# Kernel tuning notes

Hardware: AMD Instinct MI355X
Metric: run time of the kernel (lower is better)

Reference implementation:

```python
import jax, jax.numpy as jnp
import numpy as np

B, T, N_EMBD = 8, 2048, 512
N_HEAD = 4
EPS = 1e-5
NEG_INF = -1e9


def setup_inputs() -> dict:
    key = jax.random.key(0)
    ks = jax.random.split(key, 10)
    x = jax.random.normal(ks[0], (B, T, N_EMBD), dtype=jnp.float32)
    # relative-position index map [t, t] into a (2t-1)-entry boolean mask table
    pos_emb = jax.random.randint(ks[1], (T, T), 0, 2 * T - 1)
    ln_w = jax.random.normal(ks[2], (N_EMBD,), dtype=jnp.float32) * 0.02 + 1.0
    ln_b = jax.random.normal(ks[3], (N_EMBD,), dtype=jnp.float32) * 0.02
    aff_w = jax.random.normal(ks[4], (N_EMBD,), dtype=jnp.float32) * 0.02 + 1.0
    aff_b = jax.random.normal(ks[5], (N_EMBD,), dtype=jnp.float32) * 0.02
    W_qkv = jax.random.normal(ks[6], (N_EMBD, 3 * N_EMBD), dtype=jnp.float32) * (N_EMBD ** -0.5)
    # boolean lookup table; True = position visible (mostly visible)
    mask_table = jax.random.uniform(ks[7], (2 * T - 1,)) > 0.2
    W_proj = jax.random.normal(ks[8], (N_EMBD, N_EMBD), dtype=jnp.float32) * (N_EMBD ** -0.5)
    return {
        "x": x, "pos_emb": pos_emb, "ln_w": ln_w, "ln_b": ln_b,
        "aff_w": aff_w, "aff_b": aff_b, "W_qkv": W_qkv,
        "mask_table": mask_table, "W_proj": W_proj,
    }


def reference(x, pos_emb, ln_w, ln_b, aff_w, aff_b, W_qkv, mask_table, W_proj):
    b, t, n = x.shape
    hd = n // N_HEAD
    # LayerNorm (mean subtract, rms normalize, affine)
    x = x - jnp.mean(x, axis=-1, keepdims=True)
    x = x * jax.lax.rsqrt(jnp.mean(x * x, axis=-1, keepdims=True) + EPS)
    x = x * ln_w + ln_b
    # extra affine (onnx initializers 7/8) then fused QKV projection
    x = x * aff_w + aff_b
    qkv = x @ W_qkv                       # [b, t, 3n]
    q, k, v = jnp.split(qkv, 3, axis=2)
    q = q.reshape(b, t, N_HEAD, hd).transpose(0, 2, 1, 3)  # [b, h, t, hd]
    k = k.reshape(b, t, N_HEAD, hd).transpose(0, 2, 1, 3)
    v = v.reshape(b, t, N_HEAD, hd).transpose(0, 2, 1, 3)
    scale = 1.0 / np.sqrt(hd).astype(np.float32)
    scores = jnp.einsum('bhqd,bhkd->bhqk', q, k) * scale   # [b, h, t, t]
    # gather-based relative-position mask: True = attend, False = mask out
    mask = mask_table[pos_emb]                             # [t, t] bool
    scores = jnp.where(mask, scores, NEG_INF)
    attn = jax.nn.softmax(scores, axis=-1)
    out = jnp.einsum('bhqk,bhkd->bhqd', attn, v)           # [b, h, t, hd]
    out = out.transpose(0, 2, 1, 3).reshape(b, t, n)
    return out @ W_proj
```

## Files before the change

kernel.cpp:

```cpp
#include <hip/hip_runtime.h>
#include <hip/hip_bf16.h>

#define T_SEQ 2048
#define NEMBD 512
#define NHEAD 4
#define HDIM  128
#define BATCH 8
#define MROWS (BATCH * T_SEQ)
#define QSCALE 0.12751744534f

typedef __attribute__((ext_vector_type(8))) short short8;
typedef __attribute__((ext_vector_type(4))) short short4v;
typedef __attribute__((ext_vector_type(4))) float f32x4;

static __device__ __forceinline__ float bf2f(unsigned short h) {
  return __uint_as_float(((unsigned int)h) << 16);
}
static __device__ __forceinline__ short f2bs(float f) {
  unsigned int u = __float_as_uint(f);
  unsigned int r = (u + 0x7FFFu + ((u >> 16) & 1u)) >> 16;
  return (short)r;
}
static __device__ __forceinline__ unsigned int pk2(float a, float b) {
  __hip_bfloat162 h = __float22bfloat162_rn(make_float2(a, b));
  return *reinterpret_cast<unsigned int*>(&h);
}
static __device__ __forceinline__ int mask_at(const void* mt, int fmt, int idx) {
  if (fmt == 0) return ((const int*)mt)[idx] != 0;
  if (fmt == 1) return ((const unsigned char*)mt)[idx] != 0;
  if (fmt == 2) return ((const float*)mt)[idx] != 0.0f;
  return ((const unsigned short*)mt)[idx] != 0;
}
static __device__ __forceinline__ int pos_at(const int* pos, int i64, size_t idx) {
  return i64 ? pos[idx * 2] : pos[idx];
}
static __device__ __forceinline__ void gload16(const void* g, void* l) {
  __builtin_amdgcn_global_load_lds((const __attribute__((address_space(1))) void*)g,
                                   (__attribute__((address_space(3))) void*)l,
                                   16, 0, 0);
}

__global__ __launch_bounds__(256) void detect_kernel(
    const unsigned int* __restrict__ mt, const unsigned int* __restrict__ posw,
    int* __restrict__ flags)
{
  __shared__ int s01, sf, sbf, szero;
  const int t = threadIdx.x;
  if (t == 0) { s01 = 1; sf = 1; sbf = 1; szero = 0; }
  __syncthreads();
  int a01 = 1, af = 1, ab = 1, zc = 0;
  for (int i = t; i < 1023; i += 256) {
    const unsigned int v = mt[i];
    if (v > 1u) a01 = 0;
    const float f = __uint_as_float(v);
    if (!(f == 0.0f || f == 1.0f)) af = 0;
    const unsigned int lo = v & 0xFFFFu, hi = v >> 16;
    if (!((lo == 0u || lo == 0x3F80u) && (hi == 0u || hi == 0x3F80u))) ab = 0;
  }
  for (int i = t; i < 512; i += 256) if (posw[2 * i + 1] == 0u) zc++;
  if (!a01) atomicAnd(&s01, 0);
  if (!af)  atomicAnd(&sf, 0);
  if (!ab)  atomicAnd(&sbf, 0);
  if (zc)   atomicAdd(&szero, zc);
  __syncthreads();
  if (t == 0) {
    flags[0] = s01 ? 0 : (sf ? 2 : (sbf ? 3 : 1));
    flags[2] = (szero > 500) ? 1 : 0;
  }
}

__global__ __launch_bounds__(256) void pack_mask_kernel(
    const int* __restrict__ pos, const void* __restrict__ mt,
    const int* __restrict__ flags, unsigned int* __restrict__ mp)
{
  const int idx = blockIdx.x * 256 + threadIdx.x;
  const int fmt = flags[0];
  const int i64 = flags[2];
  const int q = idx >> 6;
  const int wrd = idx & 63;
  const size_t base = (size_t)q * T_SEQ + wrd * 32;
  unsigned int bits = 0;
  #pragma unroll 4
  for (int j = 0; j < 32; ++j)
    bits |= (mask_at(mt, fmt, pos_at(pos, i64, base + j)) ? 1u : 0u) << j;
  mp[idx] = bits;
}

__global__ __launch_bounds__(256) void vecprep_kernel(
    const float* __restrict__ lnw, const float* __restrict__ lnb,
    const float* __restrict__ afw, const float* __restrict__ afb,
    float* __restrict__ effw, float* __restrict__ effb)
{
  const int c = blockIdx.x * 256 + threadIdx.x;
  if (c >= NEMBD) return;
  effw[c] = lnw[c] * afw[c];
  effb[c] = lnb[c] * afw[c] + afb[c];
}

__global__ __launch_bounds__(256) void wconv2_kernel(
    const float* __restrict__ Wq, const float* __restrict__ Wp,
    short* __restrict__ WqT, short* __restrict__ WpT)
{
  const int idx = blockIdx.x * 256 + threadIdx.x;
  if (idx < 1536 * 512) {
    const int n = idx >> 9, k = idx & 511;
    WqT[idx] = f2bs(Wq[(size_t)k * 1536 + n]);
  } else {
    const int j = idx - 1536 * 512;
    const int n = j >> 9, k = j & 511;
    WpT[j] = f2bs(Wp[(size_t)k * 512 + n]);
  }
}

__global__ __launch_bounds__(64) void ln_kernel(
    const float* __restrict__ x, const float* __restrict__ effw, const float* __restrict__ effb,
    short* __restrict__ xp)
{
  const int row = blockIdx.x;
  const int tid = threadIdx.x;
  const float4* p = (const float4*)(x + (size_t)row * NEMBD + tid * 8);
  const float4 a0 = p[0], a1 = p[1];
  float f[8] = {a0.x, a0.y, a0.z, a0.w, a1.x, a1.y, a1.z, a1.w};
  float s = 0.f, s2 = 0.f;
  #pragma unroll
  for (int j = 0; j < 8; ++j) { s += f[j]; s2 += f[j] * f[j]; }
  #pragma unroll
  for (int off = 1; off < 64; off <<= 1) {
    s  += __shfl_xor(s, off);
    s2 += __shfl_xor(s2, off);
  }
  const float mean = s * (1.0f / NEMBD);
  const float rstd = rsqrtf(s2 * (1.0f / NEMBD) - mean * mean + 1e-5f);
  const float4* wp = (const float4*)(effw + tid * 8);
  const float4* bp = (const float4*)(effb + tid * 8);
  const float4 w0 = wp[0], w1 = wp[1], b0 = bp[0], b1 = bp[1];
  short8 ob;
  ob[0] = f2bs((f[0] - mean) * rstd * w0.x + b0.x);
  ob[1] = f2bs((f[1] - mean) * rstd * w0.y + b0.y);
  ob[2] = f2bs((f[2] - mean) * rstd * w0.z + b0.z);
  ob[3] = f2bs((f[3] - mean) * rstd * w0.w + b0.w);
  ob[4] = f2bs((f[4] - mean) * rstd * w1.x + b1.x);
  ob[5] = f2bs((f[5] - mean) * rstd * w1.y + b1.y);
  ob[6] = f2bs((f[6] - mean) * rstd * w1.z + b1.z);
  ob[7] = f2bs((f[7] - mean) * rstd * w1.w + b1.w);
  *((short8*)(xp + (size_t)row * NEMBD + tid * 8)) = ob;
}

template<int MODE>
__global__ __launch_bounds__(256) void gemm_kernel(
    const short* __restrict__ A, const short* __restrict__ Bt,
    void* __restrict__ out0, short* __restrict__ Kp, short* __restrict__ Vt)
{
  __shared__ alignas(16) short Atile[128 * 64];
  __shared__ alignas(16) short Btile[128 * 64];
  const int tid = threadIdx.x;
  const int l = tid & 63;
  const int w = tid >> 6;
  const int m0 = blockIdx.x * 128;
  const int n0 = blockIdx.y * 128;
  const int w_r = w >> 1, w_c = w & 1;
  const int lr = l & 15, lg = l >> 4;
  f32x4 acc[4][4] = {};

  for (int kt = 0; kt < 512; kt += 64) {
    #pragma unroll
    for (int i = 0; i < 4; ++i) {
      const int c = i * 256 + tid;
      const int row = c >> 3, col8 = c & 7;
      gload16(A  + (size_t)(m0 + row) * 512 + kt + col8 * 8, Atile + (i * 256 + w * 64) * 8);
      gload16(Bt + (size_t)(n0 + row) * 512 + kt + col8 * 8, Btile + (i * 256 + w * 64) * 8);
    }
    __syncthreads();
    #pragma unroll
    for (int kk = 0; kk < 2; ++kk) {
      short8 af[4], bfm[4];
      #pragma unroll
      for (int m = 0; m < 4; ++m)
        af[m] = *(const short8*)&Atile[(w_r * 64 + m * 16 + lr) * 64 + kk * 32 + lg * 8];
      #pragma unroll
      for (int n = 0; n < 4; ++n)
        bfm[n] = *(const short8*)&Btile[(w_c * 64 + n * 16 + lr) * 64 + kk * 32 + lg * 8];
      #pragma unroll
      for (int m = 0; m < 4; ++m)
        #pragma unroll
        for (int n = 0; n < 4; ++n)
          acc[m][n] = __builtin_amdgcn_mfma_f32_16x16x32_bf16(af[m], bfm[n], acc[m][n], 0, 0, 0);
    }
    __syncthreads();
  }

  if (MODE == 1) {
    float* out = (float*)out0;
    #pragma unroll
    for (int m = 0; m < 4; ++m)
      #pragma unroll
      for (int n = 0; n < 4; ++n)
        #pragma unroll
        for (int r = 0; r < 4; ++r) {
          const int gm = m0 + w_r * 64 + m * 16 + lg * 4 + r;
          const int gn = n0 + w_c * 64 + n * 16 + lr;
          out[(size_t)gm * NEMBD + gn] = acc[m][n][r];
        }
  } else {
    const int which = n0 >> 9;
    const int h = (n0 >> 7) & 3;
    short* Qp = (short*)out0;
    #pragma unroll
    for (int m = 0; m < 4; ++m)
      #pragma unroll
      for (int n = 0; n < 4; ++n)
        #pragma unroll
        for (int r = 0; r < 4; ++r) {
          const int gm = m0 + w_r * 64 + m * 16 + lg * 4 + r;
          const int b = gm >> 11, t = gm & 2047;
          const int d = w_c * 64 + n * 16 + lr;
          const size_t bh = (size_t)((b << 2) | h);
          const float v = acc[m][n][r];
          if (which == 0)      Qp[(bh * T_SEQ + t) * HDIM + d] = f2bs(v * QSCALE);
          else if (which == 1) Kp[(bh * T_SEQ + t) * HDIM + d] = f2bs(v);
          else                 Vt[(bh * HDIM + d) * T_SEQ + t] = f2bs(v);
        }
  }
}

__global__ __launch_bounds__(512, 4) void attn_kernel(
    const short* __restrict__ Q, const short* __restrict__ Kp, const short* __restrict__ Vt,
    const unsigned int* __restrict__ maskP, short* __restrict__ O)
{
  __shared__ alignas(16) short Kt[2][32 * 128];
  __shared__ alignas(16) short Vs[2][128 * 32];
  __shared__ alignas(16) short Pw[8][16 * 40];
  const int tid = threadIdx.x;
  const int l = tid & 63;
  const int w = tid >> 6;
  const int lr = l & 15, lg = l >> 4;
  const int s7 = lr & 7;
  const int vkey = (lr >> 1) & 3;
  const int swz = ((blockIdx.x & 7) << 6) | (blockIdx.x >> 3);
  const int bh = swz >> 4;
  const int q0 = (swz & 15) * 128 + w * 16;
  const short* Qb = Q  + (size_t)bh * T_SEQ * HDIM;
  const short* Kb = Kp + (size_t)bh * T_SEQ * HDIM;
  const short* Vb = Vt + (size_t)bh * HDIM * T_SEQ;

  const int kr = tid >> 4, kc = tid & 15;
  const int vr = tid >> 2, vc = tid & 3;
  #define STAGE(b, kti) do {                                                        \
    const int kt_ = (kti) * 32;                                                     \
    gload16(Kb + (size_t)(kt_ + kr) * HDIM + (kc ^ (kr & 7)) * 8,                   \
            (char*)&Kt[b][0] + w * 1024);                                           \
    gload16(Vb + (size_t)vr * T_SEQ + kt_ + (vc ^ ((vr >> 1) & 3)) * 8,             \
            (char*)&Vs[b][0] + w * 1024);                                           \
  } while (0)

  short8 aq[4];
  #pragma unroll
  for (int kk = 0; kk < 4; ++kk)
    aq[kk] = *(const short8*)(Qb + (size_t)(q0 + lr) * HDIM + kk * 32 + lg * 8);

  float lsum = 0.f;
  f32x4 acc[8] = {};
  const size_t mrow = (size_t)(q0 + lr) * 64;

  STAGE(0, 0);
  __syncthreads();
  int cur = 0;
  for (int kti = 0; kti < 64; ++kti) {
    if (kti + 1 < 64) STAGE(cur ^ 1, kti + 1);
    const unsigned int mq = maskP[mrow + kti];
    f32x4 sn[2];
    __builtin_amdgcn_s_setprio(1);
    #pragma unroll
    for (int n = 0; n < 2; ++n) {
      f32x4 s = {};
      #pragma unroll
      for (int kk = 0; kk < 4; ++kk) {
        const short8 bk = *(const short8*)((char*)&Kt[cur][0]
            + (n * 16 + lr) * 256 + ((kk * 4 + lg) ^ s7) * 16);
        s = __builtin_amdgcn_mfma_f32_16x16x32_bf16(bk, aq[kk], s, 0, 0, 0);
      }
      sn[n] = s;
    }
    __builtin_amdgcn_s_setprio(0);
    #pragma unroll
    for (int n = 0; n < 2; ++n) {
      const int base = n * 16 + lg * 4;
      const float p0 = __builtin_amdgcn_exp2f(((mq >> (base + 0)) & 1) ? sn[n][0] : -1e9f);
      const float p1 = __builtin_amdgcn_exp2f(((mq >> (base + 1)) & 1) ? sn[n][1] : -1e9f);
      const float p2 = __builtin_amdgcn_exp2f(((mq >> (base + 2)) & 1) ? sn[n][2] : -1e9f);
      const float p3 = __builtin_amdgcn_exp2f(((mq >> (base + 3)) & 1) ? sn[n][3] : -1e9f);
      lsum += (p0 + p1) + (p2 + p3);
      union { short4v s4; unsigned int u[2]; } pwv;
      pwv.u[0] = pk2(p0, p1);
      pwv.u[1] = pk2(p2, p3);
      *(short4v*)&Pw[w][lr * 40 + base] = pwv.s4;
    }
    const short8 pa = *(const short8*)&Pw[w][lr * 40 + lg * 8];
    __builtin_amdgcn_s_setprio(1);
    #pragma unroll
    for (int nn = 0; nn < 8; ++nn) {
      const short8 bv = *(const short8*)((char*)&Vs[cur][0]
          + (nn * 16 + lr) * 64 + (lg ^ vkey) * 16);
      acc[nn] = __builtin_amdgcn_mfma_f32_16x16x32_bf16(pa, bv, acc[nn], 0, 0, 0);
    }
    __builtin_amdgcn_s_setprio(0);
    __syncthreads();
    cur ^= 1;
  }
  #undef STAGE

  float s = lsum;
  s += __shfl_xor(s, 16);
  s += __shfl_xor(s, 32);
  const float rin = 1.0f / s;
  float rin4[4];
  #pragma unroll
  for (int r = 0; r < 4; ++r) rin4[r] = __shfl(rin, lg * 4 + r);
  const int b = bh >> 2, h = bh & 3;
  #pragma unroll
  for (int nn = 0; nn < 8; ++nn) {
    const int d = nn * 16 + lr;
    #pragma unroll
    for (int r = 0; r < 4; ++r) {
      const int qg = q0 + lg * 4 + r;
      O[((size_t)b * T_SEQ + qg) * NEMBD + h * HDIM + d] = f2bs(acc[nn][r] * rin4[r]);
    }
  }
}

__global__ __launch_bounds__(256) void fill_kernel(float* __restrict__ out, float v, size_t n) {
  for (size_t i = blockIdx.x * 256 + threadIdx.x; i < n; i += (size_t)gridDim.x * 256)
    out[i] = v;
}

extern "C" void kernel_launch(void* const* d_in, const int* in_sizes, int n_in,
                              void* d_out, int out_size, void* d_ws, size_t ws_size,
                              hipStream_t stream)
{
  const float* x     = (const float*)d_in[0];
  const int*   pos   = (const int*)d_in[1];
  const float* lnw   = (const float*)d_in[2];
  const float* lnb   = (const float*)d_in[3];
  const float* afw   = (const float*)d_in[4];
  const float* afb   = (const float*)d_in[5];
  const float* Wqkv  = (const float*)d_in[6];
  const void*  mtab  = d_in[7];
  const float* Wproj = (const float*)d_in[8];

  size_t off = 0;
  char* ws = (char*)d_ws;
  int* flags = (int*)(ws + off);                   off += 256;
  float* effw = (float*)(ws + off);                off += 2048;
  float* effb = (float*)(ws + off);                off += 2048;
  unsigned int* maskP = (unsigned int*)(ws + off); off += (size_t)T_SEQ * 64 * 4;
  short* Xp  = (short*)(ws + off);                 off += (size_t)MROWS * NEMBD * 2;
  short* WqT = (short*)(ws + off);                 off += (size_t)3 * NEMBD * NEMBD * 2;
  short* WpT = (short*)(ws + off);                 off += (size_t)NEMBD * NEMBD * 2;
  short* Qb  = (short*)(ws + off);                 off += (size_t)BATCH * NHEAD * T_SEQ * HDIM * 2;
  short* Kb  = (short*)(ws + off);                 off += (size_t)BATCH * NHEAD * T_SEQ * HDIM * 2;
  short* Vt  = (short*)(ws + off);                 off += (size_t)BATCH * NHEAD * T_SEQ * HDIM * 2;
  short* Ob  = Xp;

  if (ws_size < off) {
    fill_kernel<<<256, 256, 0, stream>>>((float*)d_out, (float)(ws_size >> 20), (size_t)out_size);
    return;
  }

  detect_kernel<<<1, 256, 0, stream>>>((const unsigned int*)mtab, (const unsigned int*)pos, flags);
  pack_mask_kernel<<<(T_SEQ * (T_SEQ / 32)) / 256, 256, 0, stream>>>(pos, mtab, flags, maskP);
  vecprep_kernel<<<2, 256, 0, stream>>>(lnw, lnb, afw, afb, effw, effb);
  wconv2_kernel<<<(4 * NEMBD * NEMBD) / 256, 256, 0, stream>>>(Wqkv, Wproj, WqT, WpT);
  ln_kernel<<<MROWS, 64, 0, stream>>>(x, effw, effb, Xp);
  dim3 g0(128, 12);
  gemm_kernel<0><<<g0, 256, 0, stream>>>(Xp, WqT, (void*)Qb, Kb, Vt);
  attn_kernel<<<512, 512, 0, stream>>>(Qb, Kb, Vt, maskP, Ob);
  dim3 g1(128, 4);
  gemm_kernel<1><<<g1, 256, 0, stream>>>(Ob, WpT, d_out, nullptr, nullptr);
}
```

Baseline: 219.9 us.

## Process two 16-row query tiles per wave in attention, halving block size

Each wave in the attention kernel now handles 32 query rows (two 16-row MFMA tiles) instead of 16, and blocks shrink from 512 to 256 threads while keeping 128 queries per block. Every K/V fragment read from LDS now feeds two MFMAs, which halves LDS read traffic per FLOP. The staging loop is rewritten so fewer threads load the same tiles. The cost is doubled accumulator and Q registers per wave, which lowers the occupancy bound from 4 to 3 blocks and may cause spilling.

```diff
diff --git a/kernel.cpp b/kernel.cpp
--- a/kernel.cpp
+++ b/kernel.cpp
@@ -223,13 +223,13 @@
   }
 }
 
-__global__ __launch_bounds__(512, 4) void attn_kernel(
+__global__ __launch_bounds__(256, 3) void attn_kernel(
     const short* __restrict__ Q, const short* __restrict__ Kp, const short* __restrict__ Vt,
     const unsigned int* __restrict__ maskP, short* __restrict__ O)
 {
   __shared__ alignas(16) short Kt[2][32 * 128];
   __shared__ alignas(16) short Vs[2][128 * 32];
-  __shared__ alignas(16) short Pw[8][16 * 40];
+  __shared__ alignas(16) short Pw[4][32 * 40];
   const int tid = threadIdx.x;
   const int l = tid & 63;
   const int w = tid >> 6;
@@ -238,70 +238,96 @@
   const int vkey = (lr >> 1) & 3;
   const int swz = ((blockIdx.x & 7) << 6) | (blockIdx.x >> 3);
   const int bh = swz >> 4;
-  const int q0 = (swz & 15) * 128 + w * 16;
+  const int q0 = (swz & 15) * 128 + w * 32;
   const short* Qb = Q  + (size_t)bh * T_SEQ * HDIM;
   const short* Kb = Kp + (size_t)bh * T_SEQ * HDIM;
   const short* Vb = Vt + (size_t)bh * HDIM * T_SEQ;
 
-  const int kr = tid >> 4, kc = tid & 15;
-  const int vr = tid >> 2, vc = tid & 3;
   #define STAGE(b, kti) do {                                                        \
     const int kt_ = (kti) * 32;                                                     \
-    gload16(Kb + (size_t)(kt_ + kr) * HDIM + (kc ^ (kr & 7)) * 8,                   \
-            (char*)&Kt[b][0] + w * 1024);                                           \
-    gload16(Vb + (size_t)vr * T_SEQ + kt_ + (vc ^ ((vr >> 1) & 3)) * 8,             \
-            (char*)&Vs[b][0] + w * 1024);                                           \
+    _Pragma("unroll")                                                               \
+    for (int i = 0; i < 2; ++i) {                                                   \
+      const int r = i * 16 + (tid >> 4);                                            \
+      gload16(Kb + (size_t)(kt_ + r) * HDIM + ((tid & 15) ^ (r & 7)) * 8,           \
+              (char*)&Kt[b][0] + i * 4096 + w * 1024);                              \
+    }                                                                               \
+    _Pragma("unroll")                                                               \
+    for (int i = 0; i < 2; ++i) {                                                   \
+      const int r = i * 64 + (tid >> 2);                                            \
+      gload16(Vb + (size_t)r * T_SEQ + kt_ + ((tid & 3) ^ ((r >> 1) & 3)) * 8,      \
+              (char*)&Vs[b][0] + i * 4096 + w * 1024);                              \
+    }                                                                               \
   } while (0)
 
-  short8 aq[4];
+  short8 aq0[4], aq1[4];
   #pragma unroll
-  for (int kk = 0; kk < 4; ++kk)
-    aq[kk] = *(const short8*)(Qb + (size_t)(q0 + lr) * HDIM + kk * 32 + lg * 8);
-
-  float lsum = 0.f;
-  f32x4 acc[8] = {};
-  const size_t mrow = (size_t)(q0 + lr) * 64;
+  for (int kk = 0; kk < 4; ++kk) {
+    aq0[kk] = *(const short8*)(Qb + (size_t)(q0 + lr) * HDIM + kk * 32 + lg * 8);
+    aq1[kk] = *(const short8*)(Qb + (size_t)(q0 + 16 + lr) * HDIM + kk * 32 + lg * 8);
+  }
+
+  float lsum0 = 0.f, lsum1 = 0.f;
+  f32x4 acc0[8] = {}, acc1[8] = {};
+  const size_t mrow0 = (size_t)(q0 + lr) * 64;
+  const size_t mrow1 = (size_t)(q0 + 16 + lr) * 64;
 
   STAGE(0, 0);
   __syncthreads();
   int cur = 0;
   for (int kti = 0; kti < 64; ++kti) {
     if (kti + 1 < 64) STAGE(cur ^ 1, kti + 1);
-    const unsigned int mq = maskP[mrow + kti];
-    f32x4 sn[2];
+    const unsigned int mq0 = maskP[mrow0 + kti];
+    const unsigned int mq1 = maskP[mrow1 + kti];
+    f32x4 sn0[2], sn1[2];
     __builtin_amdgcn_s_setprio(1);
     #pragma unroll
     for (int n = 0; n < 2; ++n) {
-      f32x4 s = {};
+      f32x4 a0 = {}, a1 = {};
       #pragma unroll
       for (int kk = 0; kk < 4; ++kk) {
         const short8 bk = *(const short8*)((char*)&Kt[cur][0]
             + (n * 16 + lr) * 256 + ((kk * 4 + lg) ^ s7) * 16);
-        s = __builtin_amdgcn_mfma_f32_16x16x32_bf16(bk, aq[kk], s, 0, 0, 0);
+        a0 = __builtin_amdgcn_mfma_f32_16x16x32_bf16(bk, aq0[kk], a0, 0, 0, 0);
+        a1 = __builtin_amdgcn_mfma_f32_16x16x32_bf16(bk, aq1[kk], a1, 0, 0, 0);
       }
-      sn[n] = s;
+      sn0[n] = a0; sn1[n] = a1;
     }
     __builtin_amdgcn_s_setprio(0);
     #pragma unroll
     for (int n = 0; n < 2; ++n) {
       const int base = n * 16 + lg * 4;
-      const float p0 = __builtin_amdgcn_exp2f(((mq >> (base + 0)) & 1) ? sn[n][0] : -1e9f);
-      const float p1 = __builtin_amdgcn_exp2f(((mq >> (base + 1)) & 1) ? sn[n][1] : -1e9f);
-      const float p2 = __builtin_amdgcn_exp2f(((mq >> (base + 2)) & 1) ? sn[n][2] : -1e9f);
-      const float p3 = __builtin_amdgcn_exp2f(((mq >> (base + 3)) & 1) ? sn[n][3] : -1e9f);
-      lsum += (p0 + p1) + (p2 + p3);
-      union { short4v s4; unsigned int u[2]; } pwv;
-      pwv.u[0] = pk2(p0, p1);
-      pwv.u[1] = pk2(p2, p3);
-      *(short4v*)&Pw[w][lr * 40 + base] = pwv.s4;
-    }
-    const short8 pa = *(const short8*)&Pw[w][lr * 40 + lg * 8];
+      {
+        const float p0 = __builtin_amdgcn_exp2f(((mq0 >> (base + 0)) & 1) ? sn0[n][0] : -1e9f);
+        const float p1 = __builtin_amdgcn_exp2f(((mq0 >> (base + 1)) & 1) ? sn0[n][1] : -1e9f);
+        const float p2 = __builtin_amdgcn_exp2f(((mq0 >> (base + 2)) & 1) ? sn0[n][2] : -1e9f);
+        const float p3 = __builtin_amdgcn_exp2f(((mq0 >> (base + 3)) & 1) ? sn0[n][3] : -1e9f);
+        lsum0 += (p0 + p1) + (p2 + p3);
+        union { short4v s4; unsigned int u[2]; } pwv;
+        pwv.u[0] = pk2(p0, p1);
+        pwv.u[1] = pk2(p2, p3);
+        *(short4v*)&Pw[w][lr * 40 + base] = pwv.s4;
+      }
+      {
+        const float p0 = __builtin_amdgcn_exp2f(((mq1 >> (base + 0)) & 1) ? sn1[n][0] : -1e9f);
+        const float p1 = __builtin_amdgcn_exp2f(((mq1 >> (base + 1)) & 1) ? sn1[n][1] : -1e9f);
+        const float p2 = __builtin_amdgcn_exp2f(((mq1 >> (base + 2)) & 1) ? sn1[n][2] : -1e9f);
+        const float p3 = __builtin_amdgcn_exp2f(((mq1 >> (base + 3)) & 1) ? sn1[n][3] : -1e9f);
+        lsum1 += (p0 + p1) + (p2 + p3);
+        union { short4v s4; unsigned int u[2]; } pwv;
+        pwv.u[0] = pk2(p0, p1);
+        pwv.u[1] = pk2(p2, p3);
+        *(short4v*)&Pw[w][(16 + lr) * 40 + base] = pwv.s4;
+      }
+    }
+    const short8 pa0 = *(const short8*)&Pw[w][lr * 40 + lg * 8];
+    const short8 pa1 = *(const short8*)&Pw[w][(16 + lr) * 40 + lg * 8];
     __builtin_amdgcn_s_setprio(1);
     #pragma unroll
     for (int nn = 0; nn < 8; ++nn) {
       const short8 bv = *(const short8*)((char*)&Vs[cur][0]
           + (nn * 16 + lr) * 64 + (lg ^ vkey) * 16);
-      acc[nn] = __builtin_amdgcn_mfma_f32_16x16x32_bf16(pa, bv, acc[nn], 0, 0, 0);
+      acc0[nn] = __builtin_amdgcn_mfma_f32_16x16x32_bf16(pa0, bv, acc0[nn], 0, 0, 0);
+      acc1[nn] = __builtin_amdgcn_mfma_f32_16x16x32_bf16(pa1, bv, acc1[nn], 0, 0, 0);
     }
     __builtin_amdgcn_s_setprio(0);
     __syncthreads();
@@ -309,21 +335,26 @@
   }
   #undef STAGE
 
-  float s = lsum;
-  s += __shfl_xor(s, 16);
-  s += __shfl_xor(s, 32);
-  const float rin = 1.0f / s;
-  float rin4[4];
+  float s0 = lsum0, s1 = lsum1;
+  s0 += __shfl_xor(s0, 16); s0 += __shfl_xor(s0, 32);
+  s1 += __shfl_xor(s1, 16); s1 += __shfl_xor(s1, 32);
+  const float rin0 = 1.0f / s0;
+  const float rin1 = 1.0f / s1;
+  float rin40[4], rin41[4];
   #pragma unroll
-  for (int r = 0; r < 4; ++r) rin4[r] = __shfl(rin, lg * 4 + r);
+  for (int r = 0; r < 4; ++r) {
+    rin40[r] = __shfl(rin0, lg * 4 + r);
+    rin41[r] = __shfl(rin1, lg * 4 + r);
+  }
   const int b = bh >> 2, h = bh & 3;
   #pragma unroll
   for (int nn = 0; nn < 8; ++nn) {
     const int d = nn * 16 + lr;
     #pragma unroll
     for (int r = 0; r < 4; ++r) {
-      const int qg = q0 + lg * 4 + r;
-      O[((size_t)b * T_SEQ + qg) * NEMBD + h * HDIM + d] = f2bs(acc[nn][r] * rin4[r]);
+      const int qg0 = q0 + lg * 4 + r;
+      O[((size_t)b * T_SEQ + qg0) * NEMBD + h * HDIM + d] = f2bs(acc0[nn][r] * rin40[r]);
+      O[((size_t)b * T_SEQ + qg0 + 16) * NEMBD + h * HDIM + d] = f2bs(acc1[nn][r] * rin41[r]);
     }
   }
 }
@@ -373,7 +404,7 @@
   ln_kernel<<<MROWS, 64, 0, stream>>>(x, effw, effb, Xp);
   dim3 g0(128, 12);
   gemm_kernel<0><<<g0, 256, 0, stream>>>(Xp, WqT, (void*)Qb, Kb, Vt);
-  attn_kernel<<<512, 512, 0, stream>>>(Qb, Kb, Vt, maskP, Ob);
+  attn_kernel<<<512, 256, 0, stream>>>(Qb, Kb, Vt, maskP, Ob);
   dim3 g1(128, 4);
   gemm_kernel<1><<<g1, 256, 0, stream>>>(Ob, WpT, d_out, nullptr, nullptr);
 }
```

Result: slower. 227.5 us (+3.4%).
